# Optimization experiments

Measured on AMD Instinct MI355X. Metric: run time of the kernel, lower is better.

The kernel has to match this reference:

```python
import jax, jax.numpy as jnp
import numpy as np

D_MODEL = 1024
NUM_HEADS = 16
HEAD_DIM = D_MODEL // NUM_HEADS
B, L = 2, 2048


def setup_inputs() -> dict:
    key = jax.random.key(0)
    ks = jax.random.split(key, 9)
    s = 0.02
    return {
        "query": jax.random.normal(ks[0], (B, L, D_MODEL), dtype=jnp.float32),
        "key": jax.random.normal(ks[1], (B, L, D_MODEL), dtype=jnp.float32),
        "value": jax.random.normal(ks[2], (B, L, D_MODEL), dtype=jnp.float32),
        "mask": jax.random.randint(ks[3], (B, L), 0, 2, dtype=jnp.int32),
        "Wq": jax.random.normal(ks[4], (D_MODEL, D_MODEL), dtype=jnp.float32) * s,
        "Wk": jax.random.normal(ks[5], (D_MODEL, D_MODEL), dtype=jnp.float32) * s,
        "Wv": jax.random.normal(ks[6], (D_MODEL, D_MODEL), dtype=jnp.float32) * s,
        "Wo": jax.random.normal(ks[7], (D_MODEL, D_MODEL), dtype=jnp.float32) * s,
        "bo": jnp.zeros((D_MODEL,), dtype=jnp.float32),
    }


def _split_heads(x):
    # (B, L, d_model) -> (B, H, L, head_dim)
    b, l, _ = x.shape
    return x.reshape(b, l, NUM_HEADS, HEAD_DIM).transpose(0, 2, 1, 3)


def reference(query, key, value, mask, Wq, Wk, Wv, Wo, bo):
    # nn.Linear(bias=False): x @ W.T
    q = _split_heads(query @ Wq.T)   # (B, H, L, hd)
    k = _split_heads(key @ Wk.T)
    v = _split_heads(value @ Wv.T)

    scores = jnp.einsum("bhqd,bhkd->bhqk", q, k) / jnp.sqrt(jnp.float32(HEAD_DIM))
    # padding mask over keys: (B, L) -> (B, 1, 1, L); 0 = pad -> -inf
    keep = (mask[:, None, None, :] != 0)
    scores = jnp.where(keep, scores, -jnp.inf)

    attn = jax.nn.softmax(scores, axis=-1)
    # original zeroes NaN rows (fully-masked query rows)
    attn = jnp.where(jnp.isnan(attn), jnp.zeros_like(attn), attn)
    # dropout is identity in eval/reference mode

    ctx = jnp.einsum("bhqk,bhkd->bhqd", attn, v)           # (B, H, L, hd)
    ctx = ctx.transpose(0, 2, 1, 3).reshape(B, L, D_MODEL)  # combine heads
    return ctx @ Wo.T + bo
```

## Files before the change

### kernel.cpp

```cpp
#include <hip/hip_runtime.h>

typedef unsigned short u16;
typedef __bf16 bf16x8 __attribute__((ext_vector_type(8)));
typedef __bf16 bf16x4 __attribute__((ext_vector_type(4)));
typedef float floatx4 __attribute__((ext_vector_type(4)));
typedef u16 u16x4 __attribute__((ext_vector_type(4)));

#define MEG ((size_t)(1u << 20))

__device__ __forceinline__ u16 f2bf(float f) {
  unsigned int u = __float_as_uint(f);
  u += 0x7fffu + ((u >> 16) & 1u);
  return (u16)(u >> 16);
}

__device__ __forceinline__ void load_lds16(const u16* g, u16* l) {
  __builtin_amdgcn_global_load_lds((const __attribute__((address_space(1))) unsigned int*)g,
                                   (__attribute__((address_space(3))) unsigned int*)l,
                                   16, 0, 0);
}

__global__ __launch_bounds__(256) void cvt7(
    const float* __restrict__ s0, const float* __restrict__ s1,
    const float* __restrict__ s2, const float* __restrict__ s3,
    const float* __restrict__ s4, const float* __restrict__ s5,
    const float* __restrict__ s6, u16* __restrict__ dst)
{
  size_t e = ((size_t)blockIdx.x * 256 + threadIdx.x) * 16;
  unsigned m = (unsigned)(e >> 20);
  const float* s; size_t off;
  if (m < 4)       { s = s0; off = e; }
  else if (m < 8)  { s = s1; off = e - 4 * MEG; }
  else if (m < 12) { s = s2; off = e - 8 * MEG; }
  else if (m < 13) { s = s3; off = e - 12 * MEG; }
  else if (m < 14) { s = s4; off = e - 13 * MEG; }
  else if (m < 15) { s = s5; off = e - 14 * MEG; }
  else             { s = s6; off = e - 15 * MEG; }
  float4 f[4];
#pragma unroll
  for (int t = 0; t < 4; ++t)
    f[t] = *reinterpret_cast<const float4*>(s + off + t * 4);
#pragma unroll
  for (int t = 0; t < 4; ++t) {
    u16x4 o;
    o.x = f2bf(f[t].x); o.y = f2bf(f[t].y); o.z = f2bf(f[t].z); o.w = f2bf(f[t].w);
    *reinterpret_cast<u16x4*>(dst + e + t * 4) = o;
  }
}

__global__ __launch_bounds__(256) void gemm_proj(
    const u16* __restrict__ Abase, const u16* __restrict__ Bbase,
    u16* __restrict__ Cbase, u16* __restrict__ VtB,
    int K, long zA, long zB, long zC)
{
  __shared__ __align__(16) u16 As[128 * 64];
  __shared__ __align__(16) u16 Bs[128 * 64];
  const int tid = threadIdx.x;
  const int w = tid >> 6, ln = tid & 63;
  const int lm = ln & 15, lq = ln >> 4;
  const int wm = w >> 1, wn = w & 1;
  const long m0 = (long)blockIdx.x * 128, n0 = (long)blockIdx.y * 128;
  const u16* A = Abase + (size_t)blockIdx.z * (size_t)zA;
  const u16* B = Bbase + (size_t)blockIdx.z * (size_t)zB;

  const int r0 = tid >> 3;
  const int kc = (tid & 7) ^ (r0 & 7);
  const u16* gA = A + (m0 + r0) * (long)K + kc * 8;
  const u16* gB = B + (n0 + r0) * (long)K + kc * 8;
  const long rstep = 32L * K;

  const int sl0 = (lq ^ (lm & 7)) * 8;
  const int sl1 = ((4 + lq) ^ (lm & 7)) * 8;
  const u16* ab0 = &As[(wm * 64 + lm) * 64 + sl0];
  const u16* ab1 = &As[(wm * 64 + lm) * 64 + sl1];
  const u16* bb0 = &Bs[(wn * 64 + lm) * 64 + sl0];
  const u16* bb1 = &Bs[(wn * 64 + lm) * 64 + sl1];

  const floatx4 z4 = {0.f, 0.f, 0.f, 0.f};
  floatx4 acc[4][4];
#pragma unroll
  for (int i = 0; i < 4; ++i)
#pragma unroll
    for (int j = 0; j < 4; ++j) acc[i][j] = z4;

  for (int k0 = 0; k0 < K; k0 += 64) {
#pragma unroll
    for (int t = 0; t < 4; ++t) {
      load_lds16(gA + t * rstep, &As[(t * 256 + w * 64) * 8]);
      load_lds16(gB + t * rstep, &Bs[(t * 256 + w * 64) * 8]);
    }
    gA += 64; gB += 64;
    __syncthreads();
    bf16x8 af[4][2], bfr[4][2];
#pragma unroll
    for (int i = 0; i < 4; ++i) {
      af[i][0] = *reinterpret_cast<const bf16x8*>(ab0 + i * 1024);
      af[i][1] = *reinterpret_cast<const bf16x8*>(ab1 + i * 1024);
    }
#pragma unroll
    for (int j = 0; j < 4; ++j) {
      bfr[j][0] = *reinterpret_cast<const bf16x8*>(bb0 + j * 1024);
      bfr[j][1] = *reinterpret_cast<const bf16x8*>(bb1 + j * 1024);
    }
#pragma unroll
    for (int i = 0; i < 4; ++i)
#pragma unroll
      for (int j = 0; j < 4; ++j) {
        acc[i][j] = __builtin_amdgcn_mfma_f32_16x16x32_bf16(af[i][0], bfr[j][0], acc[i][j], 0, 0, 0);
        acc[i][j] = __builtin_amdgcn_mfma_f32_16x16x32_bf16(af[i][1], bfr[j][1], acc[i][j], 0, 0, 0);
      }
    __syncthreads();
  }

  if (blockIdx.z == 2) {
#pragma unroll
    for (int i = 0; i < 4; ++i) {
      long row = m0 + wm * 64 + i * 16 + lq * 4;
      int bq = (int)(row >> 11);
      int l  = (int)(row & 2047);
#pragma unroll
      for (int j = 0; j < 4; ++j) {
        long col = n0 + wn * 64 + j * 16 + lm;
        int hh = (int)(col >> 6), dd = (int)(col & 63);
        u16x4 o;
        o.x = f2bf(acc[i][j][0]); o.y = f2bf(acc[i][j][1]);
        o.z = f2bf(acc[i][j][2]); o.w = f2bf(acc[i][j][3]);
        *reinterpret_cast<u16x4*>(&VtB[((size_t)(bq * 16 + hh)) * 131072 +
                                       (size_t)dd * 2048 + l]) = o;
      }
    }
    return;
  }

#pragma unroll
  for (int i = 0; i < 4; ++i) {
    long row = m0 + wm * 64 + i * 16 + lq * 4;
#pragma unroll
    for (int j = 0; j < 4; ++j) {
      long col = n0 + wn * 64 + j * 16 + lm;
#pragma unroll
      for (int r = 0; r < 4; ++r) {
        size_t idx = (size_t)(row + r) * 1024 + (size_t)col;
        (Cbase + (size_t)blockIdx.z * (size_t)zC)[idx] = f2bf(acc[i][j][r]);
      }
    }
  }
}

__global__ __launch_bounds__(256) void gemm_out_fused(
    const u16* __restrict__ OpA, const u16* __restrict__ OpB,
    const float* __restrict__ psA, const float* __restrict__ psB,
    const u16* __restrict__ Wo, const float* __restrict__ bias,
    float* __restrict__ Cout)
{
  __shared__ __align__(16) u16 As[64 * 64];
  __shared__ __align__(16) u16 Bs[128 * 64];
  const int tid = threadIdx.x;
  const int w = tid >> 6, ln = tid & 63;
  const int lm = ln & 15, lq = ln >> 4;
  const int wm = w >> 1, wn = w & 1;
  const long m0 = (long)blockIdx.x * 64, n0 = (long)blockIdx.y * 128;

  const int r0 = tid >> 3;
  const int kc = (tid & 7) ^ (r0 & 7);
  const u16* gB = Wo + (n0 + r0) * 1024 + kc * 8;
  const long rstep = 32L * 1024;

  const int sl0 = (lq ^ (lm & 7)) * 8;
  const int sl1 = ((4 + lq) ^ (lm & 7)) * 8;
  const u16* ab0 = &As[(wm * 32 + lm) * 64 + sl0];
  const u16* ab1 = &As[(wm * 32 + lm) * 64 + sl1];
  const u16* bb0 = &Bs[(wn * 64 + lm) * 64 + sl0];
  const u16* bb1 = &Bs[(wn * 64 + lm) * 64 + sl1];

  int rowg[2]; int qlb[2];
#pragma unroll
  for (int t = 0; t < 2; ++t) {
    rowg[t] = (int)m0 + r0 + t * 32;
    int b = rowg[t] >> 11, l = rowg[t] & 2047;
    qlb[t] = (b << 4) * 2048 + l;
  }

  const floatx4 z4 = {0.f, 0.f, 0.f, 0.f};
  floatx4 acc[2][4];
#pragma unroll
  for (int i = 0; i < 2; ++i)
#pragma unroll
    for (int j = 0; j < 4; ++j) acc[i][j] = z4;

  for (int k0 = 0; k0 < 1024; k0 += 64) {
#pragma unroll
    for (int t = 0; t < 4; ++t)
      load_lds16(gB + t * rstep, &Bs[(t * 256 + w * 64) * 8]);
    gB += 64;
    const int h = k0 >> 6;
#pragma unroll
    for (int t = 0; t < 2; ++t) {
      int ql = qlb[t] + h * 2048;
      float s = psA[ql] + psB[ql];
      float inv = (s > 0.f) ? __builtin_amdgcn_rcpf(s) : 0.f;
      size_t idx = (size_t)rowg[t] * 1024 + k0 + kc * 8;
      uint4 ua = *reinterpret_cast<const uint4*>(OpA + idx);
      uint4 ub = *reinterpret_cast<const uint4*>(OpB + idx);
      uint4 uo;
      const unsigned* pa = reinterpret_cast<const unsigned*>(&ua);
      const unsigned* pb = reinterpret_cast<const unsigned*>(&ub);
      unsigned* po = reinterpret_cast<unsigned*>(&uo);
#pragma unroll
      for (int i = 0; i < 4; ++i) {
        float alo = __uint_as_float(pa[i] << 16);
        float ahi = __uint_as_float(pa[i] & 0xFFFF0000u);
        float blo = __uint_as_float(pb[i] << 16);
        float bhi = __uint_as_float(pb[i] & 0xFFFF0000u);
        float olo = (alo + blo) * inv;
        float ohi = (ahi + bhi) * inv;
        po[i] = (unsigned)f2bf(olo) | ((unsigned)f2bf(ohi) << 16);
      }
      *reinterpret_cast<uint4*>(&As[(size_t)(t * 256 + tid) * 8]) = uo;
    }
    __syncthreads();
    bf16x8 af[2][2], bfr[4][2];
#pragma unroll
    for (int i = 0; i < 2; ++i) {
      af[i][0] = *reinterpret_cast<const bf16x8*>(ab0 + i * 1024);
      af[i][1] = *reinterpret_cast<const bf16x8*>(ab1 + i * 1024);
    }
#pragma unroll
    for (int j = 0; j < 4; ++j) {
      bfr[j][0] = *reinterpret_cast<const bf16x8*>(bb0 + j * 1024);
      bfr[j][1] = *reinterpret_cast<const bf16x8*>(bb1 + j * 1024);
    }
#pragma unroll
    for (int i = 0; i < 2; ++i)
#pragma unroll
      for (int j = 0; j < 4; ++j) {
        acc[i][j] = __builtin_amdgcn_mfma_f32_16x16x32_bf16(af[i][0], bfr[j][0], acc[i][j], 0, 0, 0);
        acc[i][j] = __builtin_amdgcn_mfma_f32_16x16x32_bf16(af[i][1], bfr[j][1], acc[i][j], 0, 0, 0);
      }
    __syncthreads();
  }

#pragma unroll
  for (int i = 0; i < 2; ++i) {
    long row = m0 + wm * 32 + i * 16 + lq * 4;
#pragma unroll
    for (int j = 0; j < 4; ++j) {
      long col = n0 + wn * 64 + j * 16 + lm;
      float bv = bias[col];
#pragma unroll
      for (int r = 0; r < 4; ++r)
        Cout[(size_t)(row + r) * 1024 + (size_t)col] = acc[i][j][r] + bv;
    }
  }
}

__global__ __launch_bounds__(256, 4) void attn_kernel(
    const u16* __restrict__ Qp, const u16* __restrict__ Kp,
    const u16* __restrict__ Vt, const int* __restrict__ mask,
    u16* __restrict__ OpBase, float* __restrict__ psAB)
{
  __shared__ __align__(16) u16 Ks[64 * 64];
  __shared__ __align__(16) u16 Vts[64 * 64];
  __shared__ __align__(16) u16 Ps[4 * 32 * 64];
  __shared__ __align__(16) float mball[1024];

  const int tid = threadIdx.x;
  const int w = tid >> 6, ln = tid & 63;
  const int lm = ln & 15, lq = ln >> 4;
  const int bh = blockIdx.y, b = bh >> 4, h = bh & 15;
  const int q0 = blockIdx.x * 128;
  const int kz = blockIdx.z;

  const u16* Qh = Qp + (size_t)b * 2048 * 1024 + h * 64;
  const u16* Kh = Kp + (size_t)b * 2048 * 1024 + (size_t)kz * 1024 * 1024 + h * 64;
  const u16* Vth = Vt + (size_t)bh * 64 * 2048 + kz * 1024;
  u16* Op = OpBase + (size_t)kz * 8 * MEG;
  float* psZ = psAB + (size_t)kz * 65536;

  const int* mrowp = mask + b * 2048 + kz * 1024;
#pragma unroll
  for (int t = 0; t < 4; ++t) {
    int i = t * 256 + tid;
    mball[i] = (mrowp[i] != 0) ? 0.f : -__builtin_inff();
  }

  bf16x8 qf[2][2];
#pragma unroll
  for (int m = 0; m < 2; ++m) {
    int qrow = q0 + w * 32 + m * 16 + lm;
    qf[m][0] = *reinterpret_cast<const bf16x8*>(Qh + (size_t)qrow * 1024 + lq * 8);
    qf[m][1] = *reinterpret_cast<const bf16x8*>(Qh + (size_t)qrow * 1024 + 32 + lq * 8);
  }

  const int sl0 = (lq ^ (lm & 7)) * 8;
  const int sl1 = ((4 + lq) ^ (lm & 7)) * 8;
  const u16* kb0 = &Ks[lm * 64 + sl0];
  const u16* kb1 = &Ks[lm * 64 + sl1];
  const u16* vb0 = &Vts[lm * 64 + sl0];
  const u16* vb1 = &Vts[lm * 64 + sl1];
  u16* Pw = &Ps[w * 2048];
  u16* pwr[4];
#pragma unroll
  for (int n = 0; n < 4; ++n) pwr[n] = &Pw[lm * 64 + (((4 * n + lq) ^ lm) * 4)];
  const u16* prd[4];
#pragma unroll
  for (int t = 0; t < 4; ++t)
    prd[t] = &Pw[lm * 64 + (((8 * (t >> 1) + 2 * lq + (t & 1)) ^ lm) * 4)];
  const float* mbi = mball + lq * 4;

  const int r0 = tid >> 3;
  const int kc = (tid & 7) ^ (r0 & 7);
  const u16* gK0 = Kh + (size_t)r0 * 1024 + kc * 8;
  const u16* gK1 = gK0 + 32 * 1024;
  const u16* gV0 = Vth + (size_t)r0 * 2048 + kc * 8;
  const u16* gV1 = gV0 + 32 * 2048;

  const floatx4 z4 = {0.f, 0.f, 0.f, 0.f};
  floatx4 O[2][4];
#pragma unroll
  for (int m = 0; m < 2; ++m)
#pragma unroll
    for (int j = 0; j < 4; ++j) O[m][j] = z4;
  float psum[2] = {0.f, 0.f};
  const float SCL = 0.18033688011112042f;

  for (int it = 0; it < 16; ++it) {
    load_lds16(gK0, &Ks[(w * 64) * 8]);
    load_lds16(gK1, &Ks[(256 + w * 64) * 8]);
    load_lds16(gV0, &Vts[(w * 64) * 8]);
    load_lds16(gV1, &Vts[(256 + w * 64) * 8]);
    gK0 += 64 * 1024; gK1 += 64 * 1024; gV0 += 64; gV1 += 64;
    __syncthreads();

    bf16x8 kf[4][2], vf[4][2];
#pragma unroll
    for (int n = 0; n < 4; ++n) {
      kf[n][0] = *reinterpret_cast<const bf16x8*>(kb0 + n * 1024);
      kf[n][1] = *reinterpret_cast<const bf16x8*>(kb1 + n * 1024);
    }
#pragma unroll
    for (int j = 0; j < 4; ++j) {
      vf[j][0] = *reinterpret_cast<const bf16x8*>(vb0 + j * 1024);
      vf[j][1] = *reinterpret_cast<const bf16x8*>(vb1 + j * 1024);
    }
    float4 mb4[4];
#pragma unroll
    for (int n = 0; n < 4; ++n)
      mb4[n] = *reinterpret_cast<const float4*>(mbi + n * 16);
    mbi += 64;

#pragma unroll
    for (int m = 0; m < 2; ++m) {
      floatx4 S[4];
#pragma unroll
      for (int n = 0; n < 4; ++n) {
        S[n] = __builtin_amdgcn_mfma_f32_16x16x32_bf16(kf[n][0], qf[m][0], z4, 0, 0, 0);
        S[n] = __builtin_amdgcn_mfma_f32_16x16x32_bf16(kf[n][1], qf[m][1], S[n], 0, 0, 0);
      }

#pragma unroll
      for (int n = 0; n < 4; ++n) {
        float p0 = __builtin_amdgcn_exp2f(fmaf(S[n][0], SCL, mb4[n].x));
        float p1 = __builtin_amdgcn_exp2f(fmaf(S[n][1], SCL, mb4[n].y));
        float p2 = __builtin_amdgcn_exp2f(fmaf(S[n][2], SCL, mb4[n].z));
        float p3 = __builtin_amdgcn_exp2f(fmaf(S[n][3], SCL, mb4[n].w));
        psum[m] += (p0 + p1) + (p2 + p3);
        unsigned u0 = __float_as_uint(p0) + 0x8000u;
        unsigned u1 = __float_as_uint(p1) + 0x8000u;
        unsigned u2 = __float_as_uint(p2) + 0x8000u;
        unsigned u3 = __float_as_uint(p3) + 0x8000u;
        uint2 pk;
        pk.x = __builtin_amdgcn_perm(u1, u0, 0x07060302u);
        pk.y = __builtin_amdgcn_perm(u3, u2, 0x07060302u);
        *reinterpret_cast<uint2*>(pwr[n] + m * 1024) = pk;
      }

#pragma unroll
      for (int h2 = 0; h2 < 2; ++h2) {
        bf16x4 pa = *reinterpret_cast<const bf16x4*>(prd[2 * h2] + m * 1024);
        bf16x4 pb = *reinterpret_cast<const bf16x4*>(prd[2 * h2 + 1] + m * 1024);
        bf16x8 pf = __builtin_shufflevector(pa, pb, 0, 1, 2, 3, 4, 5, 6, 7);
#pragma unroll
        for (int j = 0; j < 4; ++j)
          O[m][j] = __builtin_amdgcn_mfma_f32_16x16x32_bf16(pf, vf[j][h2], O[m][j], 0, 0, 0);
      }
    }
    __syncthreads();
  }

#pragma unroll
  for (int m = 0; m < 2; ++m) {
    float s = psum[m];
    s += __shfl_xor(s, 16, 64);
    s += __shfl_xor(s, 32, 64);
    int prow = q0 + w * 32 + m * 16 + lm;
    if (lq == 0) psZ[bh * 2048 + prow] = s;
#pragma unroll
    for (int r = 0; r < 4; ++r) {
      int row = q0 + w * 32 + m * 16 + lq * 4 + r;
      size_t base = ((size_t)b * 2048 + row) * 1024 + h * 64 + lm;
#pragma unroll
      for (int j = 0; j < 4; ++j)
        Op[base + j * 16] = f2bf(O[m][j][r]);
    }
  }
}

extern "C" void kernel_launch(void* const* d_in, const int* in_sizes, int n_in,
                              void* d_out, int out_size, void* d_ws, size_t ws_size,
                              hipStream_t stream) {
  const float* q  = (const float*)d_in[0];
  const float* k  = (const float*)d_in[1];
  const float* v  = (const float*)d_in[2];
  const int*   mk = (const int*)  d_in[3];
  const float* wq = (const float*)d_in[4];
  const float* wk = (const float*)d_in[5];
  const float* wv = (const float*)d_in[6];
  const float* wo = (const float*)d_in[7];
  const float* bo = (const float*)d_in[8];

  u16* ws16 = (u16*)d_ws;
  u16* Xq  = ws16;
  u16* Wq  = ws16 + 12 * MEG;
  u16* Wo  = ws16 + 15 * MEG;
  u16* Qp  = ws16 + 16 * MEG;
  u16* Kp  = ws16 + 20 * MEG;
  u16* Vt  = ws16 + 24 * MEG;
  u16* OpA = ws16;
  u16* OpB = ws16 + 8 * MEG;
  float* psAB = (float*)(ws16 + 12 * MEG);

  cvt7<<<dim3(4096), dim3(256), 0, stream>>>(q, k, v, wq, wk, wv, wo, ws16);

  gemm_proj<<<dim3(32, 8, 3), dim3(256), 0, stream>>>(
      Xq, Wq, Qp, Vt, 1024, (long)(4 * MEG), (long)MEG, (long)(4 * MEG));

  attn_kernel<<<dim3(16, 32, 2), dim3(256), 0, stream>>>(Qp, Kp, Vt, mk, OpA, psAB);

  gemm_out_fused<<<dim3(64, 8), dim3(256), 0, stream>>>(
      OpA, OpB, psAB, psAB + 65536, Wo, bo, (float*)d_out);
}
```

Measured before the change: 220.0 us.

## Double-buffer K/V tiles and keep P in registers via permlane swaps

Changes the attention inner loop to double-buffer the K and V LDS tiles, issuing the next tile's async global-to-LDS loads before computing on the current one and dropping one barrier per iteration. The P-matrix LDS round trip is replaced by hardware bf16 pack conversion plus permlane32/permlane16 swaps that rearrange the probabilities into the MFMA A-operand layout directly in registers. It also adds s_setprio around the MFMA groups. LDS use grows for the doubled K/V buffers while the P buffer goes away. Rounding changes from round-half-up to the hardware conversion's rounding.

```diff
diff --git a/kernel.cpp b/kernel.cpp
--- a/kernel.cpp
+++ b/kernel.cpp
@@ -5,6 +5,8 @@
 typedef __bf16 bf16x4 __attribute__((ext_vector_type(4)));
 typedef float floatx4 __attribute__((ext_vector_type(4)));
 typedef u16 u16x4 __attribute__((ext_vector_type(4)));
+typedef unsigned uint32x2 __attribute__((ext_vector_type(2)));
+typedef unsigned uint32x4 __attribute__((ext_vector_type(4)));
 
 #define MEG ((size_t)(1u << 20))
 
@@ -12,6 +14,12 @@
   unsigned int u = __float_as_uint(f);
   u += 0x7fffu + ((u >> 16) & 1u);
   return (u16)(u >> 16);
+}
+
+__device__ __forceinline__ unsigned cvt_pk_bf16(float lo, float hi) {
+  unsigned r;
+  asm("v_cvt_pk_bf16_f32 %0, %1, %2" : "=v"(r) : "v"(lo), "v"(hi));
+  return r;
 }
 
 __device__ __forceinline__ void load_lds16(const u16* g, u16* l) {
@@ -259,9 +267,8 @@
     const u16* __restrict__ Vt, const int* __restrict__ mask,
     u16* __restrict__ OpBase, float* __restrict__ psAB)
 {
-  __shared__ __align__(16) u16 Ks[64 * 64];
-  __shared__ __align__(16) u16 Vts[64 * 64];
-  __shared__ __align__(16) u16 Ps[4 * 32 * 64];
+  __shared__ __align__(16) u16 Ks[2 * 64 * 64];
+  __shared__ __align__(16) u16 Vts[2 * 64 * 64];
   __shared__ __align__(16) float mball[1024];
 
   const int tid = threadIdx.x;
@@ -298,14 +305,6 @@
   const u16* kb1 = &Ks[lm * 64 + sl1];
   const u16* vb0 = &Vts[lm * 64 + sl0];
   const u16* vb1 = &Vts[lm * 64 + sl1];
-  u16* Pw = &Ps[w * 2048];
-  u16* pwr[4];
-#pragma unroll
-  for (int n = 0; n < 4; ++n) pwr[n] = &Pw[lm * 64 + (((4 * n + lq) ^ lm) * 4)];
-  const u16* prd[4];
-#pragma unroll
-  for (int t = 0; t < 4; ++t)
-    prd[t] = &Pw[lm * 64 + (((8 * (t >> 1) + 2 * lq + (t & 1)) ^ lm) * 4)];
   const float* mbi = mball + lq * 4;
 
   const int r0 = tid >> 3;
@@ -324,24 +323,35 @@
   float psum[2] = {0.f, 0.f};
   const float SCL = 0.18033688011112042f;
 
+  load_lds16(gK0, &Ks[(w * 64) * 8]);
+  load_lds16(gK1, &Ks[(256 + w * 64) * 8]);
+  load_lds16(gV0, &Vts[(w * 64) * 8]);
+  load_lds16(gV1, &Vts[(256 + w * 64) * 8]);
+  gK0 += 64 * 1024; gK1 += 64 * 1024; gV0 += 64; gV1 += 64;
+  __syncthreads();
+
   for (int it = 0; it < 16; ++it) {
-    load_lds16(gK0, &Ks[(w * 64) * 8]);
-    load_lds16(gK1, &Ks[(256 + w * 64) * 8]);
-    load_lds16(gV0, &Vts[(w * 64) * 8]);
-    load_lds16(gV1, &Vts[(256 + w * 64) * 8]);
-    gK0 += 64 * 1024; gK1 += 64 * 1024; gV0 += 64; gV1 += 64;
-    __syncthreads();
+    const int cur = it & 1;
+    if (it < 15) {
+      const int nx = (cur ^ 1) * 4096;
+      load_lds16(gK0, &Ks[nx + (w * 64) * 8]);
+      load_lds16(gK1, &Ks[nx + (256 + w * 64) * 8]);
+      load_lds16(gV0, &Vts[nx + (w * 64) * 8]);
+      load_lds16(gV1, &Vts[nx + (256 + w * 64) * 8]);
+      gK0 += 64 * 1024; gK1 += 64 * 1024; gV0 += 64; gV1 += 64;
+    }
+    const int bofs = cur * 4096;
 
     bf16x8 kf[4][2], vf[4][2];
 #pragma unroll
     for (int n = 0; n < 4; ++n) {
-      kf[n][0] = *reinterpret_cast<const bf16x8*>(kb0 + n * 1024);
-      kf[n][1] = *reinterpret_cast<const bf16x8*>(kb1 + n * 1024);
+      kf[n][0] = *reinterpret_cast<const bf16x8*>(kb0 + bofs + n * 1024);
+      kf[n][1] = *reinterpret_cast<const bf16x8*>(kb1 + bofs + n * 1024);
     }
 #pragma unroll
     for (int j = 0; j < 4; ++j) {
-      vf[j][0] = *reinterpret_cast<const bf16x8*>(vb0 + j * 1024);
-      vf[j][1] = *reinterpret_cast<const bf16x8*>(vb1 + j * 1024);
+      vf[j][0] = *reinterpret_cast<const bf16x8*>(vb0 + bofs + j * 1024);
+      vf[j][1] = *reinterpret_cast<const bf16x8*>(vb1 + bofs + j * 1024);
     }
     float4 mb4[4];
 #pragma unroll
@@ -352,37 +362,42 @@
 #pragma unroll
     for (int m = 0; m < 2; ++m) {
       floatx4 S[4];
+      __builtin_amdgcn_s_setprio(1);
 #pragma unroll
       for (int n = 0; n < 4; ++n) {
         S[n] = __builtin_amdgcn_mfma_f32_16x16x32_bf16(kf[n][0], qf[m][0], z4, 0, 0, 0);
         S[n] = __builtin_amdgcn_mfma_f32_16x16x32_bf16(kf[n][1], qf[m][1], S[n], 0, 0, 0);
       }
-
-#pragma unroll
-      for (int n = 0; n < 4; ++n) {
-        float p0 = __builtin_amdgcn_exp2f(fmaf(S[n][0], SCL, mb4[n].x));
-        float p1 = __builtin_amdgcn_exp2f(fmaf(S[n][1], SCL, mb4[n].y));
-        float p2 = __builtin_amdgcn_exp2f(fmaf(S[n][2], SCL, mb4[n].z));
-        float p3 = __builtin_amdgcn_exp2f(fmaf(S[n][3], SCL, mb4[n].w));
-        psum[m] += (p0 + p1) + (p2 + p3);
-        unsigned u0 = __float_as_uint(p0) + 0x8000u;
-        unsigned u1 = __float_as_uint(p1) + 0x8000u;
-        unsigned u2 = __float_as_uint(p2) + 0x8000u;
-        unsigned u3 = __float_as_uint(p3) + 0x8000u;
-        uint2 pk;
-        pk.x = __builtin_amdgcn_perm(u1, u0, 0x07060302u);
-        pk.y = __builtin_amdgcn_perm(u3, u2, 0x07060302u);
-        *reinterpret_cast<uint2*>(pwr[n] + m * 1024) = pk;
-      }
+      __builtin_amdgcn_s_setprio(0);
 
 #pragma unroll
       for (int h2 = 0; h2 < 2; ++h2) {
-        bf16x4 pa = *reinterpret_cast<const bf16x4*>(prd[2 * h2] + m * 1024);
-        bf16x4 pb = *reinterpret_cast<const bf16x4*>(prd[2 * h2 + 1] + m * 1024);
-        bf16x8 pf = __builtin_shufflevector(pa, pb, 0, 1, 2, 3, 4, 5, 6, 7);
+        unsigned cc[2][2];
+#pragma unroll
+        for (int nn = 0; nn < 2; ++nn) {
+          const int n = 2 * h2 + nn;
+          float p0 = __builtin_amdgcn_exp2f(fmaf(S[n][0], SCL, mb4[n].x));
+          float p1 = __builtin_amdgcn_exp2f(fmaf(S[n][1], SCL, mb4[n].y));
+          float p2 = __builtin_amdgcn_exp2f(fmaf(S[n][2], SCL, mb4[n].z));
+          float p3 = __builtin_amdgcn_exp2f(fmaf(S[n][3], SCL, mb4[n].w));
+          psum[m] += (p0 + p1) + (p2 + p3);
+          cc[nn][0] = cvt_pk_bf16(p0, p1);
+          cc[nn][1] = cvt_pk_bf16(p2, p3);
+        }
+        unsigned W[4];
+#pragma unroll
+        for (int j = 0; j < 2; ++j) {
+          uint32x2 t1 = __builtin_amdgcn_permlane32_swap(cc[0][j], cc[1][j], false, false);
+          uint32x2 t2 = __builtin_amdgcn_permlane16_swap(t1.x, t1.y, false, false);
+          W[j] = t2.x; W[2 + j] = t2.y;
+        }
+        uint32x4 wv = {W[0], W[1], W[2], W[3]};
+        bf16x8 pf = __builtin_bit_cast(bf16x8, wv);
+        __builtin_amdgcn_s_setprio(1);
 #pragma unroll
         for (int j = 0; j < 4; ++j)
           O[m][j] = __builtin_amdgcn_mfma_f32_16x16x32_bf16(pf, vf[j][h2], O[m][j], 0, 0, 0);
+        __builtin_amdgcn_s_setprio(0);
       }
     }
     __syncthreads();
```

Measured after the change: 444.4 us. 102% more time.
